# Performance work log

Measured on AMD Instinct MI355X. Metric: run time of the kernel, lower is better.

## Reference

```python
import jax, jax.numpy as jnp
import numpy as np

DIM = 2048
NUM_HEADS = 16
NUM_KV_HEADS = 4
HEAD_DIM = DIM // NUM_HEADS  # 128
ROPE_BASE = 10000.0
BATCH = 2
SEQLEN = 2048


def _rms_norm(x):
    # F.rms_norm over last dim, no weight; torch default eps = dtype eps
    eps = jnp.finfo(x.dtype).eps
    ms = jnp.mean(jnp.square(x), axis=-1, keepdims=True)
    return x * jax.lax.rsqrt(ms + eps)


def _rotary_cos_sin(seqlen, dtype):
    # Rotary(head_dim, base): inv_freq over even indices, freqs = t outer inv_freq
    inv_freq = 1.0 / (ROPE_BASE ** (jnp.arange(0, HEAD_DIM, 2, dtype=jnp.float32) / HEAD_DIM))
    t = jnp.arange(seqlen, dtype=jnp.float32)
    freqs = jnp.outer(t, inv_freq)  # [T, HEAD_DIM//2]
    return jnp.cos(freqs).astype(dtype), jnp.sin(freqs).astype(dtype)


def _apply_rotary_emb(x, cos, sin):
    # x: [B, H, T, D]; split halves (modded-nanogpt style)
    d = x.shape[-1] // 2
    x1, x2 = x[..., :d], x[..., d:]
    y1 = x1 * cos + x2 * sin
    y2 = -x1 * sin + x2 * cos
    return jnp.concatenate([y1, y2], axis=-1)


def setup_inputs() -> dict:
    key = jax.random.key(0)
    ks = jax.random.split(key, 6)
    kv_dim = NUM_KV_HEADS * HEAD_DIM
    s_in = 1.0 / np.sqrt(DIM)
    return {
        "x": jax.random.normal(ks[0], (BATCH, SEQLEN, DIM), dtype=jnp.float32),
        "q_gain": jax.random.uniform(ks[1], (NUM_HEADS,), dtype=jnp.float32, minval=0.5, maxval=1.5),
        "W_q": jax.random.normal(ks[2], (DIM, DIM), dtype=jnp.float32) * s_in,
        "W_k": jax.random.normal(ks[3], (kv_dim, DIM), dtype=jnp.float32) * s_in,
        "W_v": jax.random.normal(ks[4], (kv_dim, DIM), dtype=jnp.float32) * s_in,
        "W_proj": jax.random.normal(ks[5], (DIM, DIM), dtype=jnp.float32) * s_in,
    }


def reference(x, q_gain, W_q, W_k, W_v, W_proj):
    B, T, D = x.shape
    # QKV projections (Linear with weight [out, in])
    q = (x @ W_q.T).reshape(B, T, NUM_HEADS, HEAD_DIM).transpose(0, 2, 1, 3)   # [B,H,T,d]
    k = (x @ W_k.T).reshape(B, T, NUM_KV_HEADS, HEAD_DIM).transpose(0, 2, 1, 3)
    v = (x @ W_v.T).reshape(B, T, NUM_KV_HEADS, HEAD_DIM).transpose(0, 2, 1, 3)
    # dual RMSNorm on q/k
    q = _rms_norm(q)
    k = _rms_norm(k)
    # RoPE
    cos, sin = _rotary_cos_sin(T, q.dtype)
    q = _apply_rotary_emb(q, cos, sin)
    k = _apply_rotary_emb(k, cos, sin)
    # per-head gain on q
    q = q * q_gain.astype(q.dtype)[None, :, None, None]
    # GQA: repeat kv heads to match query heads
    g = NUM_HEADS // NUM_KV_HEADS
    k = jnp.repeat(k, g, axis=1)
    v = jnp.repeat(v, g, axis=1)
    # causal scaled dot product attention
    scale = 1.0 / np.sqrt(HEAD_DIM)
    scores = jnp.einsum('bhqd,bhkd->bhqk', q, k) * scale
    causal = jnp.tril(jnp.ones((T, T), dtype=bool))
    scores = jnp.where(causal[None, None], scores, jnp.finfo(scores.dtype).min)
    probs = jax.nn.softmax(scores, axis=-1)
    y = jnp.einsum('bhqk,bhkd->bhqd', probs, v)  # [B,H,T,d]
    y = y.transpose(0, 2, 1, 3).reshape(B, T, D)
    return y @ W_proj.T
```

## Files before the change

kernel.cpp:

```cpp
#include <hip/hip_runtime.h>
#include <hip/hip_bf16.h>

#define DIMN   2048
#define NH     16
#define NKVH   4
#define HD     128
#define KVD    512
#define NQKV   3072
#define BATCH  2
#define SEQ    2048
#define MROWS  4096
#define VOFF   2560

typedef __attribute__((ext_vector_type(8))) __bf16 bf16x8;
typedef __attribute__((ext_vector_type(4))) float floatx4;

#define BIG_NEG (-1.0e30f)

__device__ __forceinline__ short bf16rn(float f) {
  union { float f; unsigned u; } v; v.f = f;
  unsigned u = v.u;
  return (short)((u + 0x7fffu + ((u >> 16) & 1u)) >> 16);
}

__device__ __forceinline__ void async_cp16(const short* g, short* l) {
  __builtin_amdgcn_global_load_lds(
      (const __attribute__((address_space(1))) unsigned int*)g,
      (__attribute__((address_space(3))) unsigned int*)l, 16, 0, 0);
}

__global__ void f32_to_bf16_kern(const float* __restrict__ in,
                                 short* __restrict__ out, int n8) {
  int i = blockIdx.x * blockDim.x + threadIdx.x;
  if (i >= n8) return;
  float4 a = ((const float4*)in)[i * 2];
  float4 b = ((const float4*)in)[i * 2 + 1];
  short r[8];
  r[0] = bf16rn(a.x); r[1] = bf16rn(a.y); r[2] = bf16rn(a.z); r[3] = bf16rn(a.w);
  r[4] = bf16rn(b.x); r[5] = bf16rn(b.y); r[6] = bf16rn(b.z); r[7] = bf16rn(b.w);
  ((uint4*)out)[i] = *(const uint4*)r;
}

__global__ __launch_bounds__(256) void gemm_bt_as(const short* __restrict__ A,
                                                  const short* __restrict__ Bw,
                                                  float* __restrict__ C,
                                                  int N, int K) {
  __shared__ __align__(16) short As[2][128 * 32];
  __shared__ __align__(16) short Bs[2][128 * 32];
  const int t = threadIdx.x;
  const int lane = t & 63, wave = t >> 6;
  const int lrow = lane & 15, quad = lane >> 4;
  const int wr = wave >> 1, wc = wave & 1;
  const int m0 = blockIdx.y * 128, n0 = blockIdx.x * 128;

  const short* pa[2];
  const short* pb[2];
  int wi2[2];
#pragma unroll
  for (int i = 0; i < 2; i++) {
    int wi = wave * 2 + i;
    int row = wi * 16 + (lane >> 2);
    int col = ((lane & 3) ^ (row & 3)) * 8;
    pa[i] = A + (size_t)(m0 + row) * K + col;
    pb[i] = Bw + (size_t)(n0 + row) * K + col;
    wi2[i] = wi;
  }

  floatx4 acc[4][4] = {};
  const int iters = K >> 5;

#pragma unroll
  for (int i = 0; i < 2; i++) {
    async_cp16(pa[i], &As[0][wi2[i] * 512]);
    async_cp16(pb[i], &Bs[0][wi2[i] * 512]);
  }

  for (int it = 0; it < iters; it++) {
    const int cur = it & 1;
    __syncthreads();

    if (it + 1 < iters) {
      const int off = (it + 1) * 32;
#pragma unroll
      for (int i = 0; i < 2; i++) {
        async_cp16(pa[i] + off, &As[cur ^ 1][wi2[i] * 512]);
        async_cp16(pb[i] + off, &Bs[cur ^ 1][wi2[i] * 512]);
      }
    }

    bf16x8 af[4], bfr[4];
#pragma unroll
    for (int mt = 0; mt < 4; mt++) {
      int row = wr * 64 + mt * 16 + lrow;
      af[mt] = *(const bf16x8*)&As[cur][row * 32 + (quad ^ (lrow & 3)) * 8];
    }
#pragma unroll
    for (int nt = 0; nt < 4; nt++) {
      int row = wc * 64 + nt * 16 + lrow;
      bfr[nt] = *(const bf16x8*)&Bs[cur][row * 32 + (quad ^ (lrow & 3)) * 8];
    }
#pragma unroll
    for (int mt = 0; mt < 4; mt++)
#pragma unroll
      for (int nt = 0; nt < 4; nt++)
        acc[mt][nt] = __builtin_amdgcn_mfma_f32_16x16x32_bf16(af[mt], bfr[nt],
                                                              acc[mt][nt], 0, 0, 0);
  }

#pragma unroll
  for (int mt = 0; mt < 4; mt++)
#pragma unroll
    for (int nt = 0; nt < 4; nt++) {
      int row = m0 + wr * 64 + mt * 16 + quad * 4;
      int col = n0 + wc * 64 + nt * 16 + lrow;
#pragma unroll
      for (int r = 0; r < 4; r++)
        C[(size_t)(row + r) * N + col] = acc[mt][nt][r];
    }
}

__global__ __launch_bounds__(256) void rms_rope_kern(const float* __restrict__ qkv,
                                                     const float* __restrict__ gain,
                                                     short* __restrict__ qb,
                                                     short* __restrict__ kb) {
  const int t = threadIdx.x;
  const int lane = t & 63, wave = t >> 6;
  const int gw = blockIdx.x * 4 + wave;
  const int row = gw / 20, slot = gw - row * 20;
  const int pos = row & (SEQ - 1);

  const float* src = (slot < 16) ? qkv + (size_t)row * NQKV + slot * HD
                                 : qkv + (size_t)row * NQKV + DIMN + (slot - 16) * HD;
  float x1 = src[lane], x2 = src[lane + 64];

  float ss = x1 * x1 + x2 * x2;
#pragma unroll
  for (int off = 32; off > 0; off >>= 1) ss += __shfl_xor(ss, off);
  float inv = rsqrtf(ss * (1.0f / 128.0f) + 1.1920928955078125e-7f);
  x1 *= inv; x2 *= inv;
  float fr = (float)pos * exp2f((float)lane * -0.20762050593045935f);
  float s, c;
  sincosf(fr, &s, &c);
  float y1 = x1 * c + x2 * s;
  float y2 = x2 * c - x1 * s;
  if (slot < 16) {
    float g = gain[slot] * 0.12751744459132754f;
    y1 *= g; y2 *= g;
  }
  short o1 = bf16rn(y1), o2 = bf16rn(y2);
  if (slot < 16) { short* d = qb + (size_t)row * DIMN + slot * HD;        d[lane] = o1; d[lane + 64] = o2; }
  else           { short* d = kb + (size_t)row * KVD + (slot - 16) * HD;  d[lane] = o1; d[lane + 64] = o2; }
}

__global__ __launch_bounds__(256) void vT_kern(const float* __restrict__ qkv,
                                               short* __restrict__ vT) {
  __shared__ short L[64 * 68];
  const int t0 = blockIdx.x * 64, d0 = blockIdx.y * 64;
  const int b = blockIdx.z >> 2, kvh = blockIdx.z & 3;
  const int t = threadIdx.x;

#pragma unroll
  for (int p = 0; p < 4; p++) {
    int tt = p * 16 + (t >> 4);
    int dd = (t & 15) * 4;
    float4 f = *(const float4*)(qkv + (size_t)(b * SEQ + t0 + tt) * NQKV + VOFF + kvh * HD + d0 + dd);
    short s4[4] = { bf16rn(f.x), bf16rn(f.y), bf16rn(f.z), bf16rn(f.w) };
    *(ushort4*)&L[tt * 68 + dd] = *(const ushort4*)s4;
  }
  __syncthreads();

  const int dl = t >> 2;
  const int tc = (t & 3) * 16;
  short tmp[16];
#pragma unroll
  for (int j = 0; j < 16; j++) tmp[j] = L[(tc + j) * 68 + dl];
  size_t obase = (size_t)((b * NKVH + kvh) * HD + d0 + dl) * SEQ + t0 + tc;
  *(uint4*)(vT + obase)     = ((const uint4*)tmp)[0];
  *(uint4*)(vT + obase + 8) = ((const uint4*)tmp)[1];
}

__global__ __launch_bounds__(256) void attn_kern(const short* __restrict__ qb,
                                                 const short* __restrict__ kb,
                                                 const short* __restrict__ vT,
                                                 short* __restrict__ yb) {
  __shared__ __align__(16) short Ks[2][64 * 128];
  __shared__ __align__(16) short Vs[128 * 64];
  __shared__ __align__(16) short Ps[128 * 72];
  const int qp = blockIdx.x;
  const int g  = blockIdx.y;
  const int b = g >> 3, kvh = (g >> 1) & 3, hp = g & 1;
  const int h0 = kvh * 4 + hp * 2;
  const int t = threadIdx.x, lane = t & 63, wave = t >> 6;
  const int h = wave & 1, rg = wave >> 1;
  const int lrow = lane & 15, quad = lane >> 4;

  int k_row[4], k_col[4], v_row[4], v_col[4];
#pragma unroll
  for (int i = 0; i < 4; i++) {
    int wi = wave * 4 + i;
    int kr = wi * 4 + (lane >> 4);
    k_row[i] = kr; k_col[i] = ((lane & 15) ^ (kr & 7)) * 8;
    int vr = wi * 8 + (lane >> 3);
    v_row[i] = vr; v_col[i] = ((lane & 7) ^ (vr & 7)) * 8;
  }
  const short* kbase = kb + (size_t)b * SEQ * KVD + kvh * HD;
  const short* vbase = vT + (size_t)(b * NKVH + kvh) * HD * SEQ;

  for (int ph = 0; ph < 2; ph++) {
    const int qt = ph ? (31 - qp) : qp;
    const int q0 = qt * 64;

    __syncthreads();

    bf16x8 aq[2][4];
#pragma unroll
    for (int mt = 0; mt < 2; mt++) {
      const short* qrow = qb + (size_t)(b * SEQ + q0 + rg * 32 + mt * 16 + lrow) * DIMN
                             + (h0 + h) * HD;
#pragma unroll
      for (int kk = 0; kk < 4; kk++)
        aq[mt][kk] = *(const bf16x8*)(qrow + kk * 32 + quad * 8);
    }

    floatx4 O[2][8] = {};
    float mI[2][4], lI[2][4];
#pragma unroll
    for (int mt = 0; mt < 2; mt++)
#pragma unroll
      for (int r = 0; r < 4; r++) { mI[mt][r] = BIG_NEG; lI[mt][r] = 0.0f; }

#pragma unroll
    for (int i = 0; i < 4; i++)
      async_cp16(kbase + (size_t)k_row[i] * KVD + k_col[i], &Ks[0][(wave * 4 + i) * 512]);

    for (int kt = 0; kt <= qt; kt++) {
      const int cur = kt & 1;
      const int k0 = kt * 64;
      __syncthreads();

#pragma unroll
      for (int i = 0; i < 4; i++)
        async_cp16(vbase + (size_t)v_row[i] * SEQ + k0 + v_col[i], &Vs[(wave * 4 + i) * 512]);
      if (kt < qt) {
        const int kn = k0 + 64;
#pragma unroll
        for (int i = 0; i < 4; i++)
          async_cp16(kbase + (size_t)(kn + k_row[i]) * KVD + k_col[i],
                     &Ks[cur ^ 1][(wave * 4 + i) * 512]);
      }

      floatx4 S[2][4] = {};
#pragma unroll
      for (int kk = 0; kk < 4; kk++)
#pragma unroll
        for (int nt = 0; nt < 4; nt++) {
          int row = nt * 16 + lrow;
          bf16x8 bk = *(const bf16x8*)&Ks[cur][row * 128 + ((kk * 4 + quad) ^ (row & 7)) * 8];
          S[0][nt] = __builtin_amdgcn_mfma_f32_16x16x32_bf16(aq[0][kk], bk, S[0][nt], 0, 0, 0);
          S[1][nt] = __builtin_amdgcn_mfma_f32_16x16x32_bf16(aq[1][kk], bk, S[1][nt], 0, 0, 0);
        }

      if (kt == qt) {
#pragma unroll
        for (int mt = 0; mt < 2; mt++)
#pragma unroll
          for (int nt = 0; nt < 4; nt++) {
            int kj = nt * 16 + lrow;
#pragma unroll
            for (int r = 0; r < 4; r++) {
              int qi = rg * 32 + mt * 16 + quad * 4 + r;
              if (kj > qi) S[mt][nt][r] = BIG_NEG;
            }
          }
      }

#pragma unroll
      for (int mt = 0; mt < 2; mt++) {
#pragma unroll
        for (int r = 0; r < 4; r++) {
          float mx = fmaxf(fmaxf(S[mt][0][r], S[mt][1][r]), fmaxf(S[mt][2][r], S[mt][3][r]));
          mx = fmaxf(mx, __shfl_xor(mx, 1));
          mx = fmaxf(mx, __shfl_xor(mx, 2));
          mx = fmaxf(mx, __shfl_xor(mx, 4));
          mx = fmaxf(mx, __shfl_xor(mx, 8));
          float mNew = fmaxf(mI[mt][r], mx);
          float alpha = exp2f(mI[mt][r] - mNew);
          float ssum = 0.0f;
#pragma unroll
          for (int nt = 0; nt < 4; nt++) {
            float p = exp2f(S[mt][nt][r] - mNew);
            S[mt][nt][r] = p;
            ssum += p;
          }
          ssum += __shfl_xor(ssum, 1);
          ssum += __shfl_xor(ssum, 2);
          ssum += __shfl_xor(ssum, 4);
          ssum += __shfl_xor(ssum, 8);
          lI[mt][r] = lI[mt][r] * alpha + ssum;
          mI[mt][r] = mNew;
#pragma unroll
          for (int n2 = 0; n2 < 8; n2++) O[mt][n2][r] *= alpha;
        }
#pragma unroll
        for (int nt = 0; nt < 4; nt++) {
          int cwr = ((nt * 2 + (lrow >> 3)) ^ (quad * 2)) * 8 + (lrow & 7);
#pragma unroll
          for (int r = 0; r < 4; r++)
            Ps[(wave * 32 + mt * 16 + quad * 4 + r) * 72 + cwr] = bf16rn(S[mt][nt][r]);
        }
      }

      __syncthreads();

#pragma unroll
      for (int kk = 0; kk < 2; kk++) {
        int capc = ((kk * 4 + quad) ^ (2 * ((lrow >> 2) & 3))) * 8;
        bf16x8 ap0 = *(const bf16x8*)&Ps[(wave * 32 + lrow) * 72 + capc];
        bf16x8 ap1 = *(const bf16x8*)&Ps[(wave * 32 + 16 + lrow) * 72 + capc];
#pragma unroll
        for (int n2 = 0; n2 < 8; n2++) {
          int row = n2 * 16 + lrow;
          bf16x8 bv = *(const bf16x8*)&Vs[row * 64 + ((kk * 4 + quad) ^ (row & 7)) * 8];
          O[0][n2] = __builtin_amdgcn_mfma_f32_16x16x32_bf16(ap0, bv, O[0][n2], 0, 0, 0);
          O[1][n2] = __builtin_amdgcn_mfma_f32_16x16x32_bf16(ap1, bv, O[1][n2], 0, 0, 0);
        }
      }
    }

#pragma unroll
    for (int mt = 0; mt < 2; mt++)
#pragma unroll
      for (int n2 = 0; n2 < 8; n2++)
#pragma unroll
        for (int r = 0; r < 4; r++) {
          float val = O[mt][n2][r] / lI[mt][r];
          int row = q0 + rg * 32 + mt * 16 + quad * 4 + r;
          int col = (h0 + h) * HD + n2 * 16 + lrow;
          yb[(size_t)(b * SEQ + row) * DIMN + col] = bf16rn(val);
        }
  }
}

extern "C" void kernel_launch(void* const* d_in, const int* in_sizes, int n_in,
                              void* d_out, int out_size, void* d_ws, size_t ws_size,
                              hipStream_t stream) {
  const float* x      = (const float*)d_in[0];
  const float* q_gain = (const float*)d_in[1];
  const float* W_q    = (const float*)d_in[2];
  const float* W_k    = (const float*)d_in[3];
  const float* W_v    = (const float*)d_in[4];
  const float* W_proj = (const float*)d_in[5];
  float* out = (float*)d_out;
  char* ws = (char*)d_ws;

  short* xb    = (short*)(ws);
  short* wqkv  = (short*)(ws + 16777216);
  short* wproj = (short*)(ws + 29360128);
  float* qkv   = (float*)(ws + 37748736);
  short* q     = (short*)(ws + 88080384);
  short* k     = (short*)(ws + 104857600);
  short* vT    = (short*)(ws + 109051904);
  short* y     = xb;

  auto cvt = [&](const float* src, short* dst, int n) {
    int n8 = n / 8;
    f32_to_bf16_kern<<<(n8 + 255) / 256, 256, 0, stream>>>(src, dst, n8);
  };
  cvt(x, xb, MROWS * DIMN);
  cvt(W_q, wqkv, DIMN * DIMN);
  cvt(W_k, wqkv + DIMN * DIMN, KVD * DIMN);
  cvt(W_v, wqkv + DIMN * DIMN + KVD * DIMN, KVD * DIMN);
  cvt(W_proj, wproj, DIMN * DIMN);

  gemm_bt_as<<<dim3(NQKV / 128, MROWS / 128), 256, 0, stream>>>(xb, wqkv, qkv, NQKV, DIMN);
  rms_rope_kern<<<(MROWS * 20) / 4, 256, 0, stream>>>(qkv, q_gain, q, k);
  vT_kern<<<dim3(SEQ / 64, HD / 64, BATCH * NKVH), 256, 0, stream>>>(qkv, vT);
  attn_kern<<<dim3(16, 16), 256, 0, stream>>>(q, k, vT, y);
  gemm_bt_as<<<dim3(DIMN / 128, MROWS / 128), 256, 0, stream>>>(y, wproj, out, DIMN, DIMN);
}
```

Before: 390.4 us.

## Emit bf16 QKV from GEMM and split attention to one head per block

The QKV GEMM now writes bf16 instead of fp32, so the intermediate buffer and the traffic of the RMS/RoPE and V-transpose kernels are halved. The attention kernel is restructured so each block handles one query head with 64 query rows (16 per wave), doubling the grid to 512 blocks and halving P shared memory. The goal is better CU occupancy on a 256-CU part. The cost is that K/V tiles are now loaded separately per head, giving more redundant K/V loads, and the q/k values pick up an extra bf16 rounding before normalization.

```diff
diff --git a/kernel.cpp b/kernel.cpp
--- a/kernel.cpp
+++ b/kernel.cpp
@@ -1,5 +1,6 @@
 #include <hip/hip_runtime.h>
 #include <hip/hip_bf16.h>
+#include <type_traits>
 
 #define DIMN   2048
 #define NH     16
@@ -22,6 +23,11 @@
   unsigned u = v.u;
   return (short)((u + 0x7fffu + ((u >> 16) & 1u)) >> 16);
 }
+__device__ __forceinline__ float bf2f(short s) {
+  union { unsigned u; float f; } v;
+  v.u = ((unsigned)(unsigned short)s) << 16;
+  return v.f;
+}
 
 __device__ __forceinline__ void async_cp16(const short* g, short* l) {
   __builtin_amdgcn_global_load_lds(
@@ -41,9 +47,10 @@
   ((uint4*)out)[i] = *(const uint4*)r;
 }
 
+template <typename OUT>
 __global__ __launch_bounds__(256) void gemm_bt_as(const short* __restrict__ A,
                                                   const short* __restrict__ Bw,
-                                                  float* __restrict__ C,
+                                                  OUT* __restrict__ C,
                                                   int N, int K) {
   __shared__ __align__(16) short As[2][128 * 32];
   __shared__ __align__(16) short Bs[2][128 * 32];
@@ -114,12 +121,16 @@
       int row = m0 + wr * 64 + mt * 16 + quad * 4;
       int col = n0 + wc * 64 + nt * 16 + lrow;
 #pragma unroll
-      for (int r = 0; r < 4; r++)
-        C[(size_t)(row + r) * N + col] = acc[mt][nt][r];
-    }
-}
-
-__global__ __launch_bounds__(256) void rms_rope_kern(const float* __restrict__ qkv,
+      for (int r = 0; r < 4; r++) {
+        if constexpr (std::is_same<OUT, short>::value)
+          C[(size_t)(row + r) * N + col] = bf16rn(acc[mt][nt][r]);
+        else
+          C[(size_t)(row + r) * N + col] = acc[mt][nt][r];
+      }
+    }
+}
+
+__global__ __launch_bounds__(256) void rms_rope_kern(const short* __restrict__ qkv,
                                                      const float* __restrict__ gain,
                                                      short* __restrict__ qb,
                                                      short* __restrict__ kb) {
@@ -129,9 +140,9 @@
   const int row = gw / 20, slot = gw - row * 20;
   const int pos = row & (SEQ - 1);
 
-  const float* src = (slot < 16) ? qkv + (size_t)row * NQKV + slot * HD
+  const short* src = (slot < 16) ? qkv + (size_t)row * NQKV + slot * HD
                                  : qkv + (size_t)row * NQKV + DIMN + (slot - 16) * HD;
-  float x1 = src[lane], x2 = src[lane + 64];
+  float x1 = bf2f(src[lane]), x2 = bf2f(src[lane + 64]);
 
   float ss = x1 * x1 + x2 * x2;
 #pragma unroll
@@ -152,7 +163,7 @@
   else           { short* d = kb + (size_t)row * KVD + (slot - 16) * HD;  d[lane] = o1; d[lane + 64] = o2; }
 }
 
-__global__ __launch_bounds__(256) void vT_kern(const float* __restrict__ qkv,
+__global__ __launch_bounds__(256) void vT_kern(const short* __restrict__ qkv,
                                                short* __restrict__ vT) {
   __shared__ short L[64 * 68];
   const int t0 = blockIdx.x * 64, d0 = blockIdx.y * 64;
@@ -163,9 +174,8 @@
   for (int p = 0; p < 4; p++) {
     int tt = p * 16 + (t >> 4);
     int dd = (t & 15) * 4;
-    float4 f = *(const float4*)(qkv + (size_t)(b * SEQ + t0 + tt) * NQKV + VOFF + kvh * HD + d0 + dd);
-    short s4[4] = { bf16rn(f.x), bf16rn(f.y), bf16rn(f.z), bf16rn(f.w) };
-    *(ushort4*)&L[tt * 68 + dd] = *(const ushort4*)s4;
+    ushort4 v = *(const ushort4*)(qkv + (size_t)(b * SEQ + t0 + tt) * NQKV + VOFF + kvh * HD + d0 + dd);
+    *(ushort4*)&L[tt * 68 + dd] = v;
   }
   __syncthreads();
 
@@ -185,13 +195,11 @@
                                                  short* __restrict__ yb) {
   __shared__ __align__(16) short Ks[2][64 * 128];
   __shared__ __align__(16) short Vs[128 * 64];
-  __shared__ __align__(16) short Ps[128 * 72];
+  __shared__ __align__(16) short Ps[64 * 72];
   const int qp = blockIdx.x;
   const int g  = blockIdx.y;
-  const int b = g >> 3, kvh = (g >> 1) & 3, hp = g & 1;
-  const int h0 = kvh * 4 + hp * 2;
+  const int b = g >> 4, h = g & 15, kvh = h >> 2;
   const int t = threadIdx.x, lane = t & 63, wave = t >> 6;
-  const int h = wave & 1, rg = wave >> 1;
   const int lrow = lane & 15, quad = lane >> 4;
 
   int k_row[4], k_col[4], v_row[4], v_col[4];
@@ -212,22 +220,16 @@
 
     __syncthreads();
 
-    bf16x8 aq[2][4];
-#pragma unroll
-    for (int mt = 0; mt < 2; mt++) {
-      const short* qrow = qb + (size_t)(b * SEQ + q0 + rg * 32 + mt * 16 + lrow) * DIMN
-                             + (h0 + h) * HD;
-#pragma unroll
-      for (int kk = 0; kk < 4; kk++)
-        aq[mt][kk] = *(const bf16x8*)(qrow + kk * 32 + quad * 8);
-    }
-
-    floatx4 O[2][8] = {};
-    float mI[2][4], lI[2][4];
-#pragma unroll
-    for (int mt = 0; mt < 2; mt++)
-#pragma unroll
-      for (int r = 0; r < 4; r++) { mI[mt][r] = BIG_NEG; lI[mt][r] = 0.0f; }
+    bf16x8 aq[4];
+    const short* qrow = qb + (size_t)(b * SEQ + q0 + wave * 16 + lrow) * DIMN + h * HD;
+#pragma unroll
+    for (int kk = 0; kk < 4; kk++)
+      aq[kk] = *(const bf16x8*)(qrow + kk * 32 + quad * 8);
+
+    floatx4 O[8] = {};
+    float mI[4], lI[4];
+#pragma unroll
+    for (int r = 0; r < 4; r++) { mI[r] = BIG_NEG; lI[r] = 0.0f; }
 
 #pragma unroll
     for (int i = 0; i < 4; i++)
@@ -249,65 +251,60 @@
                      &Ks[cur ^ 1][(wave * 4 + i) * 512]);
       }
 
-      floatx4 S[2][4] = {};
+      floatx4 S[4] = {};
 #pragma unroll
       for (int kk = 0; kk < 4; kk++)
 #pragma unroll
         for (int nt = 0; nt < 4; nt++) {
           int row = nt * 16 + lrow;
           bf16x8 bk = *(const bf16x8*)&Ks[cur][row * 128 + ((kk * 4 + quad) ^ (row & 7)) * 8];
-          S[0][nt] = __builtin_amdgcn_mfma_f32_16x16x32_bf16(aq[0][kk], bk, S[0][nt], 0, 0, 0);
-          S[1][nt] = __builtin_amdgcn_mfma_f32_16x16x32_bf16(aq[1][kk], bk, S[1][nt], 0, 0, 0);
+          S[nt] = __builtin_amdgcn_mfma_f32_16x16x32_bf16(aq[kk], bk, S[nt], 0, 0, 0);
         }
 
       if (kt == qt) {
 #pragma unroll
-        for (int mt = 0; mt < 2; mt++)
-#pragma unroll
-          for (int nt = 0; nt < 4; nt++) {
-            int kj = nt * 16 + lrow;
-#pragma unroll
-            for (int r = 0; r < 4; r++) {
-              int qi = rg * 32 + mt * 16 + quad * 4 + r;
-              if (kj > qi) S[mt][nt][r] = BIG_NEG;
-            }
+        for (int nt = 0; nt < 4; nt++) {
+          int kj = nt * 16 + lrow;
+#pragma unroll
+          for (int r = 0; r < 4; r++) {
+            int qi = wave * 16 + quad * 4 + r;
+            if (kj > qi) S[nt][r] = BIG_NEG;
           }
-      }
-
-#pragma unroll
-      for (int mt = 0; mt < 2; mt++) {
-#pragma unroll
-        for (int r = 0; r < 4; r++) {
-          float mx = fmaxf(fmaxf(S[mt][0][r], S[mt][1][r]), fmaxf(S[mt][2][r], S[mt][3][r]));
-          mx = fmaxf(mx, __shfl_xor(mx, 1));
-          mx = fmaxf(mx, __shfl_xor(mx, 2));
-          mx = fmaxf(mx, __shfl_xor(mx, 4));
-          mx = fmaxf(mx, __shfl_xor(mx, 8));
-          float mNew = fmaxf(mI[mt][r], mx);
-          float alpha = exp2f(mI[mt][r] - mNew);
-          float ssum = 0.0f;
-#pragma unroll
-          for (int nt = 0; nt < 4; nt++) {
-            float p = exp2f(S[mt][nt][r] - mNew);
-            S[mt][nt][r] = p;
-            ssum += p;
-          }
-          ssum += __shfl_xor(ssum, 1);
-          ssum += __shfl_xor(ssum, 2);
-          ssum += __shfl_xor(ssum, 4);
-          ssum += __shfl_xor(ssum, 8);
-          lI[mt][r] = lI[mt][r] * alpha + ssum;
-          mI[mt][r] = mNew;
-#pragma unroll
-          for (int n2 = 0; n2 < 8; n2++) O[mt][n2][r] *= alpha;
         }
+      }
+
+#pragma unroll
+      for (int r = 0; r < 4; r++) {
+        float mx = fmaxf(fmaxf(S[0][r], S[1][r]), fmaxf(S[2][r], S[3][r]));
+        mx = fmaxf(mx, __shfl_xor(mx, 1));
+        mx = fmaxf(mx, __shfl_xor(mx, 2));
+        mx = fmaxf(mx, __shfl_xor(mx, 4));
+        mx = fmaxf(mx, __shfl_xor(mx, 8));
+        float mNew = fmaxf(mI[r], mx);
+        float alpha = exp2f(mI[r] - mNew);
+        float ssum = 0.0f;
 #pragma unroll
         for (int nt = 0; nt < 4; nt++) {
-          int cwr = ((nt * 2 + (lrow >> 3)) ^ (quad * 2)) * 8 + (lrow & 7);
-#pragma unroll
-          for (int r = 0; r < 4; r++)
-            Ps[(wave * 32 + mt * 16 + quad * 4 + r) * 72 + cwr] = bf16rn(S[mt][nt][r]);
+          float p = exp2f(S[nt][r] - mNew);
+          S[nt][r] = p;
+          ssum += p;
         }
+        ssum += __shfl_xor(ssum, 1);
+        ssum += __shfl_xor(ssum, 2);
+        ssum += __shfl_xor(ssum, 4);
+        ssum += __shfl_xor(ssum, 8);
+        lI[r] = lI[r] * alpha + ssum;
+        mI[r] = mNew;
+#pragma unroll
+        for (int n2 = 0; n2 < 8; n2++) O[n2][r] *= alpha;
+      }
+
+#pragma unroll
+      for (int nt = 0; nt < 4; nt++) {
+        int cwr = ((nt * 2 + (lrow >> 3)) ^ (quad * 2)) * 8 + (lrow & 7);
+#pragma unroll
+        for (int r = 0; r < 4; r++)
+          Ps[(wave * 16 + quad * 4 + r) * 72 + cwr] = bf16rn(S[nt][r]);
       }
 
       __syncthreads();
@@ -315,29 +312,25 @@
 #pragma unroll
       for (int kk = 0; kk < 2; kk++) {
         int capc = ((kk * 4 + quad) ^ (2 * ((lrow >> 2) & 3))) * 8;
-        bf16x8 ap0 = *(const bf16x8*)&Ps[(wave * 32 + lrow) * 72 + capc];
-        bf16x8 ap1 = *(const bf16x8*)&Ps[(wave * 32 + 16 + lrow) * 72 + capc];
+        bf16x8 ap = *(const bf16x8*)&Ps[(wave * 16 + lrow) * 72 + capc];
 #pragma unroll
         for (int n2 = 0; n2 < 8; n2++) {
           int row = n2 * 16 + lrow;
           bf16x8 bv = *(const bf16x8*)&Vs[row * 64 + ((kk * 4 + quad) ^ (row & 7)) * 8];
-          O[0][n2] = __builtin_amdgcn_mfma_f32_16x16x32_bf16(ap0, bv, O[0][n2], 0, 0, 0);
-          O[1][n2] = __builtin_amdgcn_mfma_f32_16x16x32_bf16(ap1, bv, O[1][n2], 0, 0, 0);
+          O[n2] = __builtin_amdgcn_mfma_f32_16x16x32_bf16(ap, bv, O[n2], 0, 0, 0);
         }
       }
     }
 
 #pragma unroll
-    for (int mt = 0; mt < 2; mt++)
-#pragma unroll
-      for (int n2 = 0; n2 < 8; n2++)
-#pragma unroll
-        for (int r = 0; r < 4; r++) {
-          float val = O[mt][n2][r] / lI[mt][r];
-          int row = q0 + rg * 32 + mt * 16 + quad * 4 + r;
-          int col = (h0 + h) * HD + n2 * 16 + lrow;
-          yb[(size_t)(b * SEQ + row) * DIMN + col] = bf16rn(val);
-        }
+    for (int n2 = 0; n2 < 8; n2++)
+#pragma unroll
+      for (int r = 0; r < 4; r++) {
+        float val = O[n2][r] / lI[r];
+        int row = q0 + wave * 16 + quad * 4 + r;
+        int col = h * HD + n2 * 16 + lrow;
+        yb[(size_t)(b * SEQ + row) * DIMN + col] = bf16rn(val);
+      }
   }
 }
 
@@ -356,10 +349,10 @@
   short* xb    = (short*)(ws);
   short* wqkv  = (short*)(ws + 16777216);
   short* wproj = (short*)(ws + 29360128);
-  float* qkv   = (float*)(ws + 37748736);
-  short* q     = (short*)(ws + 88080384);
-  short* k     = (short*)(ws + 104857600);
-  short* vT    = (short*)(ws + 109051904);
+  short* qkvb  = (short*)(ws + 37748736);
+  short* q     = (short*)(ws + 62914560);
+  short* k     = (short*)(ws + 79691776);
+  short* vT    = (short*)(ws + 83886080);
   short* y     = xb;
 
   auto cvt = [&](const float* src, short* dst, int n) {
@@ -372,9 +365,9 @@
   cvt(W_v, wqkv + DIMN * DIMN + KVD * DIMN, KVD * DIMN);
   cvt(W_proj, wproj, DIMN * DIMN);
 
-  gemm_bt_as<<<dim3(NQKV / 128, MROWS / 128), 256, 0, stream>>>(xb, wqkv, qkv, NQKV, DIMN);
-  rms_rope_kern<<<(MROWS * 20) / 4, 256, 0, stream>>>(qkv, q_gain, q, k);
-  vT_kern<<<dim3(SEQ / 64, HD / 64, BATCH * NKVH), 256, 0, stream>>>(qkv, vT);
-  attn_kern<<<dim3(16, 16), 256, 0, stream>>>(q, k, vT, y);
-  gemm_bt_as<<<dim3(DIMN / 128, MROWS / 128), 256, 0, stream>>>(y, wproj, out, DIMN, DIMN);
-}
+  gemm_bt_as<short><<<dim3(NQKV / 128, MROWS / 128), 256, 0, stream>>>(xb, wqkv, qkvb, NQKV, DIMN);
+  rms_rope_kern<<<(MROWS * 20) / 4, 256, 0, stream>>>(qkvb, q_gain, q, k);
+  vT_kern<<<dim3(SEQ / 64, HD / 64, BATCH * NKVH), 256, 0, stream>>>(qkvb, vT);
+  attn_kern<<<dim3(16, 32), 256, 0, stream>>>(q, k, vT, y);
+  gemm_bt_as<float><<<dim3(DIMN / 128, MROWS / 128), 256, 0, stream>>>(y, wproj, out, DIMN, DIMN);
+}
```

New measurement: 349.2 us. 1.12x faster.
